# Performance work log

Hardware: AMD Instinct MI355X
Metric: run time of the kernel (lower is better)

## Reference

```python
import jax, jax.numpy as jnp
import numpy as np

B, T, I, H = 32768, 18, 2, 64  # batch, seq_len (forced by fc2 in_features=18), input_dim, hidden_dim


def setup_inputs() -> dict:
    key = jax.random.key(0)
    ks = jax.random.split(key, 13)
    s = 1.0 / np.sqrt(H)  # torch default GRU/Linear init scale
    return {
        "x": jax.random.normal(ks[0], (B, T, I), jnp.float32),
        "w_ih_f": jax.random.uniform(ks[1], (3 * H, I), jnp.float32, -s, s),
        "w_hh_f": jax.random.uniform(ks[2], (3 * H, H), jnp.float32, -s, s),
        "b_ih_f": jax.random.uniform(ks[3], (3 * H,), jnp.float32, -s, s),
        "b_hh_f": jax.random.uniform(ks[4], (3 * H,), jnp.float32, -s, s),
        "w_ih_b": jax.random.uniform(ks[5], (3 * H, I), jnp.float32, -s, s),
        "w_hh_b": jax.random.uniform(ks[6], (3 * H, H), jnp.float32, -s, s),
        "b_ih_b": jax.random.uniform(ks[7], (3 * H,), jnp.float32, -s, s),
        "b_hh_b": jax.random.uniform(ks[8], (3 * H,), jnp.float32, -s, s),
        "fc1_w": jax.random.uniform(ks[9], (24, 2 * H), jnp.float32, -s, s),
        "fc1_b": jax.random.uniform(ks[10], (24,), jnp.float32, -s, s),
        "fc2_w": jax.random.uniform(ks[11], (2, T), jnp.float32, -s, s),
        "fc2_b": jax.random.uniform(ks[12], (2,), jnp.float32, -s, s),
    }


def _gru_scan(x_proj, w_hh, b_hh):
    """x_proj: (T, B, 3H) precomputed input projections. Returns (T, B, H)."""
    h0 = jnp.zeros((x_proj.shape[1], w_hh.shape[1]), x_proj.dtype)

    def step(h, xp):
        gh = h @ w_hh.T + b_hh
        i_r, i_z, i_n = jnp.split(xp, 3, axis=-1)
        h_r, h_z, h_n = jnp.split(gh, 3, axis=-1)
        r = jax.nn.sigmoid(i_r + h_r)
        z = jax.nn.sigmoid(i_z + h_z)
        n = jnp.tanh(i_n + r * h_n)
        h_new = (1 - z) * n + z * h
        return h_new, h_new

    _, hs = jax.lax.scan(step, h0, x_proj)
    return hs


def reference(x, w_ih_f, w_hh_f, b_ih_f, b_hh_f,
              w_ih_b, w_hh_b, b_ih_b, b_hh_b,
              fc1_w, fc1_b, fc2_w, fc2_b):
    # precompute input-gate projections for both directions: (T, B, 3H)
    xp_f = jnp.einsum('bti,gi->tbg', x, w_ih_f) + b_ih_f
    xp_b = jnp.einsum('bti,gi->tbg', x[:, ::-1], w_ih_b) + b_ih_b
    hf = _gru_scan(xp_f, w_hh_f, b_hh_f)           # (T, B, H)
    hb = _gru_scan(xp_b, w_hh_b, b_hh_b)[::-1]     # (T, B, H), re-aligned to forward time
    out = jnp.concatenate([hf, hb], axis=-1).transpose(1, 0, 2)  # (B, T, 2H)
    out = out @ fc1_w.T + fc1_b                    # (B, T, 24)
    out = out.reshape(out.shape[0], 24, -1)        # (B, 24, T) raw row-major reshape, as in torch
    out = out @ fc2_w.T + fc2_b                    # (B, 24, 2)
    return out
```

## Files before the change

### kernel.cpp

```cpp
#include <hip/hip_runtime.h>

#define TT 18

typedef __attribute__((ext_vector_type(8))) short short8;
typedef __attribute__((ext_vector_type(4))) float float4_t;
typedef __attribute__((ext_vector_type(2))) unsigned int uint2_t;

#if defined(__has_builtin)
#if __has_builtin(__builtin_amdgcn_exp2f)
#define FEXP2(x) __builtin_amdgcn_exp2f(x)
#else
#define FEXP2(x) exp2f(x)
#endif
#else
#define FEXP2(x) exp2f(x)
#endif

static __device__ __forceinline__ float frcp(float x){ return __builtin_amdgcn_rcpf(x); }
static __device__ __forceinline__ unsigned rne_bits(float f){
    unsigned u = __float_as_uint(f);
    return u + 0x7fffu + ((u >> 16) & 1u);
}
static __device__ __forceinline__ void bsplit(float f, unsigned &hi, unsigned &lo){
    unsigned rb = rne_bits(f);
    hi = rb >> 16;
    float fh = __uint_as_float(rb & 0xffff0000u);
    lo = rne_bits(f - fh) >> 16;
}
static __device__ __forceinline__ unsigned pack_hi16(unsigned hi_src, unsigned lo_src){
#if defined(__has_builtin)
#if __has_builtin(__builtin_amdgcn_perm)
    return __builtin_amdgcn_perm(hi_src, lo_src, 0x07060302u);
#else
    return (lo_src >> 16) | (hi_src & 0xffff0000u);
#endif
#else
    return (lo_src >> 16) | (hi_src & 0xffff0000u);
#endif
}

union U8 { short8 s; unsigned u[4]; };

#define MFMA16(A,B,C) __builtin_amdgcn_mfma_f32_16x16x32_bf16((A),(B),(C),0,0,0)

__global__ __launch_bounds__(256) void head_precompute(
    const float* __restrict__ fc1_w, const float* __restrict__ fc1_b,
    const float* __restrict__ fc2_w, const float* __restrict__ fc2_b,
    unsigned short* __restrict__ Bhi, unsigned short* __restrict__ Blo,
    float* __restrict__ Cvec)
{
    int idx = blockIdx.x * 256 + threadIdx.x;
    if (idx < 24 * 2 * 18 * 128) {
        int jg = idx & 127;
        int t  = (idx >> 7) % 18;
        int k  = (idx / 2304) & 1;
        int r  = idx / 4608;
        float acc = 0.f;
        for (int c = 0; c < 24; ++c) {
            int s = t * 24 + c - r * 18;
            if (s >= 0 && s < 18) acc += fc2_w[k * 18 + s] * fc1_w[c * 128 + jg];
        }
        unsigned hi, lo;
        bsplit(acc, hi, lo);
        Bhi[idx] = (unsigned short)hi;
        Blo[idx] = (unsigned short)lo;
    }
    if (idx < 48) {
        int k = idx & 1, r = idx >> 1;
        float acc = fc2_b[k];
        for (int s = 0; s < 18; ++s)
            acc += fc2_w[k * 18 + s] * fc1_b[(r * 18 + s) % 24];
        Cvec[idx] = acc;
    }
}

struct SMv {
    alignas(16) unsigned short hb[2][2][1024];
    alignas(16) unsigned short b2x[2][64][8];
    alignas(16) unsigned short c2a[4][4][16][8];
    alignas(16) unsigned short zero16[8];
    uint2_t x2[16][18];
    float out_acc[16][49];
};

__global__ __launch_bounds__(256, 4) void gru_mfma(
    const float* __restrict__ x,
    const float* __restrict__ w_ih_f, const float* __restrict__ w_hh_f,
    const float* __restrict__ b_ih_f, const float* __restrict__ b_hh_f,
    const float* __restrict__ w_ih_b, const float* __restrict__ w_hh_b,
    const float* __restrict__ b_ih_b, const float* __restrict__ b_hh_b,
    const unsigned short* __restrict__ Bhi, const unsigned short* __restrict__ Blo,
    const float* __restrict__ Cvec, float* __restrict__ out)
{
    __shared__ SMv sm;
    const int tid  = threadIdx.x;
    const int lane = tid & 63;
    const int jq   = tid >> 6;
    const int col  = lane & 15;
    const int quad = lane >> 4;
    const int bi   = blockIdx.x;
    const int dir  = bi >> 11;
    const int bb   = (bi & 2047) * 16;
    const bool q0  = (quad == 0);

    const float* __restrict__ wih = dir ? w_ih_b : w_ih_f;
    const float* __restrict__ whh = dir ? w_hh_b : w_hh_f;
    const float* __restrict__ bih = dir ? b_ih_b : b_ih_f;
    const float* __restrict__ bhh = dir ? b_hh_b : b_hh_f;

    const float L1 = 1.4426950408889634f;
    const float L2 = 2.8853900817779268f;

    {
        unsigned* z = (unsigned*)&sm.hb[1][0][0];
        #pragma unroll
        for (int o = 0; o < 4; ++o) z[tid + o * 256] = 0u;
        unsigned* z2 = (unsigned*)&sm.b2x[0][0][0];
        #pragma unroll
        for (int o = 0; o < 2; ++o) z2[tid + o * 256] = 0u;
        if (tid < 4) ((unsigned*)sm.zero16)[tid] = 0u;
    }
    for (int o = tid; o < 16 * 49; o += 256) ((float*)sm.out_acc)[o] = 0.f;

    for (int p = tid; p < 288; p += 256) {
        int b = p / 18, t = p % 18;
        const float* xp = x + (size_t)(bb + b) * 36 + t * 2;
        unsigned h0, l0, h1, l1;
        bsplit(xp[0], h0, l0);
        bsplit(xp[1], h1, l1);
        uint2_t s2; s2[0] = h0 | (l0 << 16); s2[1] = h1 | (l1 << 16);
        sm.x2[b][t] = s2;
    }

    if (tid < 16) {
        int tx0 = dir ? (TT - 1) : 0;
        const float* xp = x + (size_t)(bb + tid) * 36 + tx0 * 2;
        unsigned h0, l0, h1, l1;
        bsplit(xp[0], h0, l0);
        bsplit(xp[1], h1, l1);
        U8 B;
        B.u[0] = h0 | (l0 << 16);
        B.u[1] = h0 | (h1 << 16);
        B.u[2] = l1 | (h1 << 16);
        B.u[3] = 0x3F803F80u;
        *(short8*)&sm.b2x[1][tid][0] = B.s;
    }

    if (q0) {
        int g0 = jq * 16 + col;
        #pragma unroll
        for (int ty = 0; ty < 2; ++ty) {
            int g = ty * 64 + g0;
            unsigned w0h, w0l, w1h, w1l, bh, bl;
            bsplit(L1 * wih[2 * g],     w0h, w0l);
            bsplit(L1 * wih[2 * g + 1], w1h, w1l);
            bsplit(L1 * (bih[g] + bhh[g]), bh, bl);
            U8 f;
            f.u[0] = w0h | (w0h << 16);
            f.u[1] = w0l | (w1h << 16);
            f.u[2] = w1h | (w1l << 16);
            f.u[3] = bh  | (bl  << 16);
            *(short8*)&sm.c2a[jq][ty][col][0] = f.s;
        }
        {
            unsigned bh, bl;
            bsplit(L2 * bhh[128 + g0], bh, bl);
            U8 f;
            f.u[0] = 0u; f.u[1] = 0u; f.u[2] = 0u;
            f.u[3] = bh | (bl << 16);
            *(short8*)&sm.c2a[jq][2][col][0] = f.s;
        }
        {
            int g = 128 + g0;
            unsigned w0h, w0l, w1h, w1l, bh, bl;
            bsplit(L2 * wih[2 * g],     w0h, w0l);
            bsplit(L2 * wih[2 * g + 1], w1h, w1l);
            bsplit(L2 * bih[g], bh, bl);
            U8 f;
            f.u[0] = w0h | (w0h << 16);
            f.u[1] = w0l | (w1h << 16);
            f.u[2] = w1h | (w1l << 16);
            f.u[3] = bh  | (bl  << 16);
            *(short8*)&sm.c2a[jq][3][col][0] = f.s;
        }
    }

    short8 wf[3][2];
    #pragma unroll
    for (int ty = 0; ty < 3; ++ty) {
        float sc = (ty == 2) ? L2 : L1;
        int g = ty * 64 + jq * 16 + col;
        #pragma unroll
        for (int c = 0; c < 2; ++c) {
            const float* p = whh + g * 64 + c * 32 + quad * 8;
            float4_t f0 = *(const float4_t*)p;
            float4_t f1 = *(const float4_t*)(p + 4);
            short8 s;
            #pragma unroll
            for (int e = 0; e < 8; ++e) {
                float f = (e < 4) ? f0[e] : f1[e - 4];
                s[e] = (short)(rne_bits(sc * f) >> 16);
            }
            wf[ty][c] = s;
        }
    }

    const unsigned short* c2p0 = q0 ? &sm.c2a[jq][0][col][0] : sm.zero16;
    const unsigned short* c2p1 = q0 ? &sm.c2a[jq][1][col][0] : sm.zero16;
    const unsigned short* c2p2 = q0 ? &sm.c2a[jq][2][col][0] : sm.zero16;
    const unsigned short* c2p3 = q0 ? &sm.c2a[jq][3][col][0] : sm.zero16;

    float hprev[4] = {0.f, 0.f, 0.f, 0.f};

    __syncthreads();

    auto step = [&](int t, int pr, int pw) {
        short8 hfh[2];
        hfh[0] = *(const short8*)&sm.hb[pr][0][quad * 128 + col * 8];
        hfh[1] = *(const short8*)&sm.hb[pr][0][(4 + quad) * 128 + col * 8];
        short8 b2f  = *(const short8*)&sm.b2x[pr][lane][0];
        short8 c2f0 = *(const short8*)c2p0;
        short8 c2f1 = *(const short8*)c2p1;
        short8 c2f2 = *(const short8*)c2p2;
        short8 c2f3 = *(const short8*)c2p3;

        float4_t aR  = (float4_t){0.f,0.f,0.f,0.f};
        float4_t aZ  = (float4_t){0.f,0.f,0.f,0.f};
        float4_t aNH = (float4_t){0.f,0.f,0.f,0.f};
        float4_t aNX = (float4_t){0.f,0.f,0.f,0.f};
        aR  = MFMA16(wf[0][0], hfh[0], aR);
        aR  = MFMA16(wf[0][1], hfh[1], aR);
        aR  = MFMA16(c2f0,     b2f,    aR);
        aZ  = MFMA16(wf[1][0], hfh[0], aZ);
        aZ  = MFMA16(wf[1][1], hfh[1], aZ);
        aZ  = MFMA16(c2f1,     b2f,    aZ);
        aNH = MFMA16(wf[2][0], hfh[0], aNH);
        aNH = MFMA16(wf[2][1], hfh[1], aNH);
        aNH = MFMA16(c2f2,     b2f,    aNH);
        aNX = MFMA16(c2f3,     b2f,    aNX);

        unsigned rh[4], rl[4];
        #pragma unroll
        for (int reg = 0; reg < 4; ++reg) {
            float r = frcp(1.f + FEXP2(-aR[reg]));
            float z = frcp(1.f + FEXP2(-aZ[reg]));
            float a = fmaf(r, aNH[reg], aNX[reg]);
            float n = fmaf(2.f, frcp(1.f + FEXP2(-a)), -1.f);
            float hnew = fmaf(z, hprev[reg] - n, n);
            hprev[reg] = hnew;
            unsigned rb = rne_bits(hnew);
            rh[reg] = rb;
            rl[reg] = __float_as_uint(hnew - __uint_as_float(rb & 0xffff0000u));
        }
        int woff = (jq * 2 + (quad >> 1)) * 128 + col * 8 + (quad & 1) * 4;
        uint2_t dh, dl;
        dh[0] = pack_hi16(rh[1], rh[0]);
        dh[1] = pack_hi16(rh[3], rh[2]);
        dl[0] = pack_hi16(rl[1], rl[0]);
        dl[1] = pack_hi16(rl[3], rl[2]);
        *(uint2_t*)&sm.hb[pw][0][woff] = dh;
        *(uint2_t*)&sm.hb[pw][1][woff] = dl;

        if (jq == 0 && q0) {
            int tn  = (t + 1 < TT) ? (t + 1) : (TT - 1);
            int txn = dir ? (TT - 1 - tn) : tn;
            uint2_t xs = sm.x2[col][txn];
            U8 B;
            B.u[0] = xs[0];
            B.u[1] = (xs[0] & 0xffffu) | (xs[1] << 16);
            B.u[2] = (xs[1] >> 16) | (xs[1] << 16);
            B.u[3] = 0x3F803F80u;
            *(short8*)&sm.b2x[pw][lane][0] = B.s;
        }

        if (t > 0 && ((t - 1) & 3) == jq) {
            int s  = t - 1;
            int ta = dir ? (TT - 1 - s) : s;
            int base_h = 4 * (ta / 3) + ta % 3;
            int i  = col & 3;
            int rr = base_h + (i >> 1);
            int kk = i & 1;
            size_t boff = (size_t)((rr * 2 + kk) * TT + ta) * 128 + dir * 64 + quad * 8;
            short8 hA0 = *(const short8*)(Bhi + boff);
            short8 hA1 = *(const short8*)(Bhi + boff + 32);
            short8 lA0 = *(const short8*)(Blo + boff);
            short8 lA1 = *(const short8*)(Blo + boff + 32);
            short8 hfl0 = *(const short8*)&sm.hb[pr][1][quad * 128 + col * 8];
            short8 hfl1 = *(const short8*)&sm.hb[pr][1][(4 + quad) * 128 + col * 8];
            float4_t acch = (float4_t){0.f,0.f,0.f,0.f};
            acch = MFMA16(hA0, hfh[0], acch);
            acch = MFMA16(hA1, hfh[1], acch);
            acch = MFMA16(hA0, hfl0,   acch);
            acch = MFMA16(hA1, hfl1,   acch);
            acch = MFMA16(lA0, hfh[0], acch);
            acch = MFMA16(lA1, hfh[1], acch);
            if (q0) {
                #pragma unroll
                for (int reg = 0; reg < 4; ++reg) {
                    int r2 = base_h + (reg >> 1);
                    sm.out_acc[col][r2 * 2 + (reg & 1)] += acch[reg];
                }
            }
        }
        __syncthreads();
    };

    #pragma unroll 1
    for (int tt = 0; tt < 9; ++tt) {
        step(2 * tt,     1, 0);
        step(2 * tt + 1, 0, 1);
    }

    if (jq == ((TT - 1) & 3)) {
        int s  = TT - 1;
        int ta = dir ? 0 : s;
        int base_h = 4 * (ta / 3) + ta % 3;
        int i  = col & 3;
        int rr = base_h + (i >> 1);
        int kk = i & 1;
        size_t boff = (size_t)((rr * 2 + kk) * TT + ta) * 128 + dir * 64 + quad * 8;
        short8 hA0 = *(const short8*)(Bhi + boff);
        short8 hA1 = *(const short8*)(Bhi + boff + 32);
        short8 lA0 = *(const short8*)(Blo + boff);
        short8 lA1 = *(const short8*)(Blo + boff + 32);
        short8 hfh0 = *(const short8*)&sm.hb[1][0][quad * 128 + col * 8];
        short8 hfh1 = *(const short8*)&sm.hb[1][0][(4 + quad) * 128 + col * 8];
        short8 hfl0 = *(const short8*)&sm.hb[1][1][quad * 128 + col * 8];
        short8 hfl1 = *(const short8*)&sm.hb[1][1][(4 + quad) * 128 + col * 8];
        float4_t acch = (float4_t){0.f,0.f,0.f,0.f};
        acch = MFMA16(hA0, hfh0, acch);
        acch = MFMA16(hA1, hfh1, acch);
        acch = MFMA16(hA0, hfl0, acch);
        acch = MFMA16(hA1, hfl1, acch);
        acch = MFMA16(lA0, hfh0, acch);
        acch = MFMA16(lA1, hfh1, acch);
        if (q0) {
            #pragma unroll
            for (int reg = 0; reg < 4; ++reg) {
                int r2 = base_h + (reg >> 1);
                sm.out_acc[col][r2 * 2 + (reg & 1)] += acch[reg];
            }
        }
    }
    __syncthreads();

    #pragma unroll
    for (int rep = 0; rep < 3; ++rep) {
        int o = rep * 256 + tid;
        int b = o / 48, c = o % 48;
        atomicAdd(&out[(size_t)bb * 48 + o], sm.out_acc[b][c] + 0.5f * Cvec[c]);
    }
}

extern "C" void kernel_launch(void* const* d_in, const int* in_sizes, int n_in,
                              void* d_out, int out_size, void* d_ws, size_t ws_size,
                              hipStream_t stream) {
    const float* x      = (const float*)d_in[0];
    const float* w_ih_f = (const float*)d_in[1];
    const float* w_hh_f = (const float*)d_in[2];
    const float* b_ih_f = (const float*)d_in[3];
    const float* b_hh_f = (const float*)d_in[4];
    const float* w_ih_b = (const float*)d_in[5];
    const float* w_hh_b = (const float*)d_in[6];
    const float* b_ih_b = (const float*)d_in[7];
    const float* b_hh_b = (const float*)d_in[8];
    const float* fc1_w  = (const float*)d_in[9];
    const float* fc1_b  = (const float*)d_in[10];
    const float* fc2_w  = (const float*)d_in[11];
    const float* fc2_b  = (const float*)d_in[12];
    float* out  = (float*)d_out;

    float*          Cvec = (float*)d_ws;
    unsigned short* Bhi  = (unsigned short*)((char*)d_ws + 256);
    unsigned short* Blo  = Bhi + 110592;

    hipMemsetAsync(d_out, 0, (size_t)out_size * sizeof(float), stream);
    head_precompute<<<432, 256, 0, stream>>>(fc1_w, fc1_b, fc2_w, fc2_b, Bhi, Blo, Cvec);
    gru_mfma<<<4096, 256, 0, stream>>>(x, w_ih_f, w_hh_f, b_ih_f, b_hh_f,
                                       w_ih_b, w_hh_b, b_ih_b, b_hh_b,
                                       Bhi, Blo, Cvec, out);
}
```

Measured before the change: 193.6 us.

## Fuse both GRU directions per block, process 32 batch rows, drop atomics and memset

Each block now runs both directions (8 waves, 4 per direction) over 32 batch rows, with each wave handling two 16-column MFMA tiles per step. Input x is kept as fp32 in shared memory and split to bf16 hi/lo on the fly, and the gate input weights move from shared memory into registers. Per-direction partial outputs are summed in shared memory and written directly, which removes the atomicAdd and the output memset. The cost is higher register and LDS pressure per block, and occupancy may drop under 512-thread launch bounds.

```diff
diff --git a/kernel.cpp b/kernel.cpp
--- a/kernel.cpp
+++ b/kernel.cpp
@@ -4,6 +4,7 @@
 
 typedef __attribute__((ext_vector_type(8))) short short8;
 typedef __attribute__((ext_vector_type(4))) float float4_t;
+typedef __attribute__((ext_vector_type(2))) float float2_t;
 typedef __attribute__((ext_vector_type(2))) unsigned int uint2_t;
 
 #if defined(__has_builtin)
@@ -42,6 +43,18 @@
 union U8 { short8 s; unsigned u[4]; };
 
 #define MFMA16(A,B,C) __builtin_amdgcn_mfma_f32_16x16x32_bf16((A),(B),(C),0,0,0)
+
+static __device__ __forceinline__ short8 make_b2f(float x0, float x1, bool q0){
+    unsigned h0, l0, h1, l1;
+    bsplit(x0, h0, l0);
+    bsplit(x1, h1, l1);
+    U8 B;
+    B.u[0] = q0 ? (h0 | (l0 << 16)) : 0u;
+    B.u[1] = q0 ? (h0 | (h1 << 16)) : 0u;
+    B.u[2] = q0 ? (l1 | (h1 << 16)) : 0u;
+    B.u[3] = q0 ? 0x3F803F80u : 0u;
+    return B.s;
+}
 
 __global__ __launch_bounds__(256) void head_precompute(
     const float* __restrict__ fc1_w, const float* __restrict__ fc1_b,
@@ -75,15 +88,12 @@
 }
 
 struct SMv {
-    alignas(16) unsigned short hb[2][2][1024];
-    alignas(16) unsigned short b2x[2][64][8];
-    alignas(16) unsigned short c2a[4][4][16][8];
-    alignas(16) unsigned short zero16[8];
-    uint2_t x2[16][18];
-    float out_acc[16][49];
+    alignas(16) unsigned short hb[2][2][2][2048];
+    float2_t x_s[32][18];
+    float out_acc[2][32][49];
 };
 
-__global__ __launch_bounds__(256, 4) void gru_mfma(
+__global__ __launch_bounds__(512, 4) void gru_mfma(
     const float* __restrict__ x,
     const float* __restrict__ w_ih_f, const float* __restrict__ w_hh_f,
     const float* __restrict__ b_ih_f, const float* __restrict__ b_hh_f,
@@ -95,12 +105,12 @@
     __shared__ SMv sm;
     const int tid  = threadIdx.x;
     const int lane = tid & 63;
-    const int jq   = tid >> 6;
+    const int wave = tid >> 6;
+    const int dir  = wave >> 2;
+    const int jq   = wave & 3;
     const int col  = lane & 15;
     const int quad = lane >> 4;
-    const int bi   = blockIdx.x;
-    const int dir  = bi >> 11;
-    const int bb   = (bi & 2047) * 16;
+    const int bb   = blockIdx.x * 32;
     const bool q0  = (quad == 0);
 
     const float* __restrict__ wih = dir ? w_ih_b : w_ih_f;
@@ -112,77 +122,15 @@
     const float L2 = 2.8853900817779268f;
 
     {
-        unsigned* z = (unsigned*)&sm.hb[1][0][0];
-        #pragma unroll
-        for (int o = 0; o < 4; ++o) z[tid + o * 256] = 0u;
-        unsigned* z2 = (unsigned*)&sm.b2x[0][0][0];
-        #pragma unroll
-        for (int o = 0; o < 2; ++o) z2[tid + o * 256] = 0u;
-        if (tid < 4) ((unsigned*)sm.zero16)[tid] = 0u;
-    }
-    for (int o = tid; o < 16 * 49; o += 256) ((float*)sm.out_acc)[o] = 0.f;
-
-    for (int p = tid; p < 288; p += 256) {
+        unsigned* z = (unsigned*)&sm.hb[1][0][0][0];
+        #pragma unroll
+        for (int o = 0; o < 8; ++o) z[tid + o * 512] = 0u;
+    }
+    for (int o = tid; o < 2 * 32 * 49; o += 512) ((float*)sm.out_acc)[o] = 0.f;
+
+    for (int p = tid; p < 32 * 18; p += 512) {
         int b = p / 18, t = p % 18;
-        const float* xp = x + (size_t)(bb + b) * 36 + t * 2;
-        unsigned h0, l0, h1, l1;
-        bsplit(xp[0], h0, l0);
-        bsplit(xp[1], h1, l1);
-        uint2_t s2; s2[0] = h0 | (l0 << 16); s2[1] = h1 | (l1 << 16);
-        sm.x2[b][t] = s2;
-    }
-
-    if (tid < 16) {
-        int tx0 = dir ? (TT - 1) : 0;
-        const float* xp = x + (size_t)(bb + tid) * 36 + tx0 * 2;
-        unsigned h0, l0, h1, l1;
-        bsplit(xp[0], h0, l0);
-        bsplit(xp[1], h1, l1);
-        U8 B;
-        B.u[0] = h0 | (l0 << 16);
-        B.u[1] = h0 | (h1 << 16);
-        B.u[2] = l1 | (h1 << 16);
-        B.u[3] = 0x3F803F80u;
-        *(short8*)&sm.b2x[1][tid][0] = B.s;
-    }
-
-    if (q0) {
-        int g0 = jq * 16 + col;
-        #pragma unroll
-        for (int ty = 0; ty < 2; ++ty) {
-            int g = ty * 64 + g0;
-            unsigned w0h, w0l, w1h, w1l, bh, bl;
-            bsplit(L1 * wih[2 * g],     w0h, w0l);
-            bsplit(L1 * wih[2 * g + 1], w1h, w1l);
-            bsplit(L1 * (bih[g] + bhh[g]), bh, bl);
-            U8 f;
-            f.u[0] = w0h | (w0h << 16);
-            f.u[1] = w0l | (w1h << 16);
-            f.u[2] = w1h | (w1l << 16);
-            f.u[3] = bh  | (bl  << 16);
-            *(short8*)&sm.c2a[jq][ty][col][0] = f.s;
-        }
-        {
-            unsigned bh, bl;
-            bsplit(L2 * bhh[128 + g0], bh, bl);
-            U8 f;
-            f.u[0] = 0u; f.u[1] = 0u; f.u[2] = 0u;
-            f.u[3] = bh | (bl << 16);
-            *(short8*)&sm.c2a[jq][2][col][0] = f.s;
-        }
-        {
-            int g = 128 + g0;
-            unsigned w0h, w0l, w1h, w1l, bh, bl;
-            bsplit(L2 * wih[2 * g],     w0h, w0l);
-            bsplit(L2 * wih[2 * g + 1], w1h, w1l);
-            bsplit(L2 * bih[g], bh, bl);
-            U8 f;
-            f.u[0] = w0h | (w0h << 16);
-            f.u[1] = w0l | (w1h << 16);
-            f.u[2] = w1h | (w1l << 16);
-            f.u[3] = bh  | (bl  << 16);
-            *(short8*)&sm.c2a[jq][3][col][0] = f.s;
-        }
+        sm.x_s[b][t] = *(const float2_t*)(x + (size_t)(bb + b) * 36 + t * 2);
     }
 
     short8 wf[3][2];
@@ -205,103 +153,152 @@
         }
     }
 
-    const unsigned short* c2p0 = q0 ? &sm.c2a[jq][0][col][0] : sm.zero16;
-    const unsigned short* c2p1 = q0 ? &sm.c2a[jq][1][col][0] : sm.zero16;
-    const unsigned short* c2p2 = q0 ? &sm.c2a[jq][2][col][0] : sm.zero16;
-    const unsigned short* c2p3 = q0 ? &sm.c2a[jq][3][col][0] : sm.zero16;
-
-    float hprev[4] = {0.f, 0.f, 0.f, 0.f};
+    short8 c2[4];
+    {
+        int g0 = jq * 16 + col;
+        #pragma unroll
+        for (int ty = 0; ty < 2; ++ty) {
+            int g = ty * 64 + g0;
+            unsigned w0h, w0l, w1h, w1l, bh, bl;
+            bsplit(L1 * wih[2 * g],     w0h, w0l);
+            bsplit(L1 * wih[2 * g + 1], w1h, w1l);
+            bsplit(L1 * (bih[g] + bhh[g]), bh, bl);
+            U8 f;
+            f.u[0] = q0 ? (w0h | (w0h << 16)) : 0u;
+            f.u[1] = q0 ? (w0l | (w1h << 16)) : 0u;
+            f.u[2] = q0 ? (w1h | (w1l << 16)) : 0u;
+            f.u[3] = q0 ? (bh  | (bl  << 16)) : 0u;
+            c2[ty] = f.s;
+        }
+        {
+            unsigned bh, bl;
+            bsplit(L2 * bhh[128 + g0], bh, bl);
+            U8 f;
+            f.u[0] = 0u; f.u[1] = 0u; f.u[2] = 0u;
+            f.u[3] = q0 ? (bh | (bl << 16)) : 0u;
+            c2[2] = f.s;
+        }
+        {
+            int g = 128 + g0;
+            unsigned w0h, w0l, w1h, w1l, bh, bl;
+            bsplit(L2 * wih[2 * g],     w0h, w0l);
+            bsplit(L2 * wih[2 * g + 1], w1h, w1l);
+            bsplit(L2 * bih[g], bh, bl);
+            U8 f;
+            f.u[0] = q0 ? (w0h | (w0h << 16)) : 0u;
+            f.u[1] = q0 ? (w0l | (w1h << 16)) : 0u;
+            f.u[2] = q0 ? (w1h | (w1l << 16)) : 0u;
+            f.u[3] = q0 ? (bh  | (bl  << 16)) : 0u;
+            c2[3] = f.s;
+        }
+    }
+
+    float hprev[8] = {0.f,0.f,0.f,0.f,0.f,0.f,0.f,0.f};
 
     __syncthreads();
 
     auto step = [&](int t, int pr, int pw) {
-        short8 hfh[2];
-        hfh[0] = *(const short8*)&sm.hb[pr][0][quad * 128 + col * 8];
-        hfh[1] = *(const short8*)&sm.hb[pr][0][(4 + quad) * 128 + col * 8];
-        short8 b2f  = *(const short8*)&sm.b2x[pr][lane][0];
-        short8 c2f0 = *(const short8*)c2p0;
-        short8 c2f1 = *(const short8*)c2p1;
-        short8 c2f2 = *(const short8*)c2p2;
-        short8 c2f3 = *(const short8*)c2p3;
-
-        float4_t aR  = (float4_t){0.f,0.f,0.f,0.f};
-        float4_t aZ  = (float4_t){0.f,0.f,0.f,0.f};
-        float4_t aNH = (float4_t){0.f,0.f,0.f,0.f};
-        float4_t aNX = (float4_t){0.f,0.f,0.f,0.f};
-        aR  = MFMA16(wf[0][0], hfh[0], aR);
-        aR  = MFMA16(wf[0][1], hfh[1], aR);
-        aR  = MFMA16(c2f0,     b2f,    aR);
-        aZ  = MFMA16(wf[1][0], hfh[0], aZ);
-        aZ  = MFMA16(wf[1][1], hfh[1], aZ);
-        aZ  = MFMA16(c2f1,     b2f,    aZ);
-        aNH = MFMA16(wf[2][0], hfh[0], aNH);
-        aNH = MFMA16(wf[2][1], hfh[1], aNH);
-        aNH = MFMA16(c2f2,     b2f,    aNH);
-        aNX = MFMA16(c2f3,     b2f,    aNX);
-
-        unsigned rh[4], rl[4];
-        #pragma unroll
-        for (int reg = 0; reg < 4; ++reg) {
-            float r = frcp(1.f + FEXP2(-aR[reg]));
-            float z = frcp(1.f + FEXP2(-aZ[reg]));
-            float a = fmaf(r, aNH[reg], aNX[reg]);
-            float n = fmaf(2.f, frcp(1.f + FEXP2(-a)), -1.f);
-            float hnew = fmaf(z, hprev[reg] - n, n);
-            hprev[reg] = hnew;
-            unsigned rb = rne_bits(hnew);
-            rh[reg] = rb;
-            rl[reg] = __float_as_uint(hnew - __uint_as_float(rb & 0xffff0000u));
-        }
-        int woff = (jq * 2 + (quad >> 1)) * 128 + col * 8 + (quad & 1) * 4;
-        uint2_t dh, dl;
-        dh[0] = pack_hi16(rh[1], rh[0]);
-        dh[1] = pack_hi16(rh[3], rh[2]);
-        dl[0] = pack_hi16(rl[1], rl[0]);
-        dl[1] = pack_hi16(rl[3], rl[2]);
-        *(uint2_t*)&sm.hb[pw][0][woff] = dh;
-        *(uint2_t*)&sm.hb[pw][1][woff] = dl;
-
-        if (jq == 0 && q0) {
-            int tn  = (t + 1 < TT) ? (t + 1) : (TT - 1);
-            int txn = dir ? (TT - 1 - tn) : tn;
-            uint2_t xs = sm.x2[col][txn];
-            U8 B;
-            B.u[0] = xs[0];
-            B.u[1] = (xs[0] & 0xffffu) | (xs[1] << 16);
-            B.u[2] = (xs[1] >> 16) | (xs[1] << 16);
-            B.u[3] = 0x3F803F80u;
-            *(short8*)&sm.b2x[pw][lane][0] = B.s;
-        }
-
-        if (t > 0 && ((t - 1) & 3) == jq) {
+        const bool myturn = (t > 0) && (((t - 1) & 3) == jq);
+        const int tx = dir ? (TT - 1 - t) : t;
+
+        short8 h0c0 = *(const short8*)&sm.hb[pr][dir][0][quad * 256 + col * 8];
+        short8 h0c1 = *(const short8*)&sm.hb[pr][dir][0][(4 + quad) * 256 + col * 8];
+        short8 h1c0 = *(const short8*)&sm.hb[pr][dir][0][quad * 256 + (16 + col) * 8];
+        short8 h1c1 = *(const short8*)&sm.hb[pr][dir][0][(4 + quad) * 256 + (16 + col) * 8];
+
+        float2_t xv0 = sm.x_s[col][tx];
+        float2_t xv1 = sm.x_s[16 + col][tx];
+        short8 b2f0 = make_b2f(xv0[0], xv0[1], q0);
+        short8 b2f1 = make_b2f(xv1[0], xv1[1], q0);
+
+        short8 hA0, hA1, lA0, lA1, l0c0, l0c1, l1c0, l1c1;
+        int base_h = 0;
+        if (myturn) {
             int s  = t - 1;
             int ta = dir ? (TT - 1 - s) : s;
-            int base_h = 4 * (ta / 3) + ta % 3;
+            base_h = 4 * (ta / 3) + ta % 3;
             int i  = col & 3;
             int rr = base_h + (i >> 1);
             int kk = i & 1;
             size_t boff = (size_t)((rr * 2 + kk) * TT + ta) * 128 + dir * 64 + quad * 8;
-            short8 hA0 = *(const short8*)(Bhi + boff);
-            short8 hA1 = *(const short8*)(Bhi + boff + 32);
-            short8 lA0 = *(const short8*)(Blo + boff);
-            short8 lA1 = *(const short8*)(Blo + boff + 32);
-            short8 hfl0 = *(const short8*)&sm.hb[pr][1][quad * 128 + col * 8];
-            short8 hfl1 = *(const short8*)&sm.hb[pr][1][(4 + quad) * 128 + col * 8];
-            float4_t acch = (float4_t){0.f,0.f,0.f,0.f};
-            acch = MFMA16(hA0, hfh[0], acch);
-            acch = MFMA16(hA1, hfh[1], acch);
-            acch = MFMA16(hA0, hfl0,   acch);
-            acch = MFMA16(hA1, hfl1,   acch);
-            acch = MFMA16(lA0, hfh[0], acch);
-            acch = MFMA16(lA1, hfh[1], acch);
-            if (q0) {
-                #pragma unroll
-                for (int reg = 0; reg < 4; ++reg) {
-                    int r2 = base_h + (reg >> 1);
-                    sm.out_acc[col][r2 * 2 + (reg & 1)] += acch[reg];
+            hA0 = *(const short8*)(Bhi + boff);
+            hA1 = *(const short8*)(Bhi + boff + 32);
+            lA0 = *(const short8*)(Blo + boff);
+            lA1 = *(const short8*)(Blo + boff + 32);
+            l0c0 = *(const short8*)&sm.hb[pr][dir][1][quad * 256 + col * 8];
+            l0c1 = *(const short8*)&sm.hb[pr][dir][1][(4 + quad) * 256 + col * 8];
+            l1c0 = *(const short8*)&sm.hb[pr][dir][1][quad * 256 + (16 + col) * 8];
+            l1c1 = *(const short8*)&sm.hb[pr][dir][1][(4 + quad) * 256 + (16 + col) * 8];
+        }
+
+        #pragma unroll
+        for (int nt = 0; nt < 2; ++nt) {
+            short8 hc0 = nt ? h1c0 : h0c0;
+            short8 hc1 = nt ? h1c1 : h0c1;
+            short8 b2f = nt ? b2f1 : b2f0;
+            float4_t aR  = (float4_t){0.f,0.f,0.f,0.f};
+            float4_t aZ  = (float4_t){0.f,0.f,0.f,0.f};
+            float4_t aNH = (float4_t){0.f,0.f,0.f,0.f};
+            float4_t aNX = (float4_t){0.f,0.f,0.f,0.f};
+            aR  = MFMA16(wf[0][0], hc0, aR);
+            aR  = MFMA16(wf[0][1], hc1, aR);
+            aR  = MFMA16(c2[0],    b2f, aR);
+            aZ  = MFMA16(wf[1][0], hc0, aZ);
+            aZ  = MFMA16(wf[1][1], hc1, aZ);
+            aZ  = MFMA16(c2[1],    b2f, aZ);
+            aNH = MFMA16(wf[2][0], hc0, aNH);
+            aNH = MFMA16(wf[2][1], hc1, aNH);
+            aNH = MFMA16(c2[2],    b2f, aNH);
+            aNX = MFMA16(c2[3],    b2f, aNX);
+
+            unsigned rh[4], rl[4];
+            #pragma unroll
+            for (int reg = 0; reg < 4; ++reg) {
+                float r = frcp(1.f + FEXP2(-aR[reg]));
+                float z = frcp(1.f + FEXP2(-aZ[reg]));
+                float a = fmaf(r, aNH[reg], aNX[reg]);
+                float n = fmaf(2.f, frcp(1.f + FEXP2(-a)), -1.f);
+                float hnew = fmaf(z, hprev[nt * 4 + reg] - n, n);
+                hprev[nt * 4 + reg] = hnew;
+                unsigned rb = rne_bits(hnew);
+                rh[reg] = rb;
+                rl[reg] = __float_as_uint(hnew - __uint_as_float(rb & 0xffff0000u));
+            }
+            int woff = (jq * 2 + (quad >> 1)) * 256 + (nt * 16 + col) * 8 + (quad & 1) * 4;
+            uint2_t dh, dl;
+            dh[0] = pack_hi16(rh[1], rh[0]);
+            dh[1] = pack_hi16(rh[3], rh[2]);
+            dl[0] = pack_hi16(rl[1], rl[0]);
+            dl[1] = pack_hi16(rl[3], rl[2]);
+            *(uint2_t*)&sm.hb[pw][dir][0][woff] = dh;
+            *(uint2_t*)&sm.hb[pw][dir][1][woff] = dl;
+
+            if (nt == 0 && myturn) {
+                float4_t a0 = (float4_t){0.f,0.f,0.f,0.f};
+                a0 = MFMA16(hA0, h0c0, a0);
+                a0 = MFMA16(hA1, h0c1, a0);
+                a0 = MFMA16(hA0, l0c0, a0);
+                a0 = MFMA16(hA1, l0c1, a0);
+                a0 = MFMA16(lA0, h0c0, a0);
+                a0 = MFMA16(lA1, h0c1, a0);
+                float4_t a1 = (float4_t){0.f,0.f,0.f,0.f};
+                a1 = MFMA16(hA0, h1c0, a1);
+                a1 = MFMA16(hA1, h1c1, a1);
+                a1 = MFMA16(hA0, l1c0, a1);
+                a1 = MFMA16(hA1, l1c1, a1);
+                a1 = MFMA16(lA0, h1c0, a1);
+                a1 = MFMA16(lA1, h1c1, a1);
+                if (q0) {
+                    #pragma unroll
+                    for (int reg = 0; reg < 4; ++reg) {
+                        int cell = (base_h + (reg >> 1)) * 2 + (reg & 1);
+                        sm.out_acc[dir][col][cell]      += a0[reg];
+                        sm.out_acc[dir][16 + col][cell] += a1[reg];
+                    }
                 }
             }
         }
+
         __syncthreads();
     };
 
@@ -323,22 +320,25 @@
         short8 hA1 = *(const short8*)(Bhi + boff + 32);
         short8 lA0 = *(const short8*)(Blo + boff);
         short8 lA1 = *(const short8*)(Blo + boff + 32);
-        short8 hfh0 = *(const short8*)&sm.hb[1][0][quad * 128 + col * 8];
-        short8 hfh1 = *(const short8*)&sm.hb[1][0][(4 + quad) * 128 + col * 8];
-        short8 hfl0 = *(const short8*)&sm.hb[1][1][quad * 128 + col * 8];
-        short8 hfl1 = *(const short8*)&sm.hb[1][1][(4 + quad) * 128 + col * 8];
-        float4_t acch = (float4_t){0.f,0.f,0.f,0.f};
-        acch = MFMA16(hA0, hfh0, acch);
-        acch = MFMA16(hA1, hfh1, acch);
-        acch = MFMA16(hA0, hfl0, acch);
-        acch = MFMA16(hA1, hfl1, acch);
-        acch = MFMA16(lA0, hfh0, acch);
-        acch = MFMA16(lA1, hfh1, acch);
-        if (q0) {
-            #pragma unroll
-            for (int reg = 0; reg < 4; ++reg) {
-                int r2 = base_h + (reg >> 1);
-                sm.out_acc[col][r2 * 2 + (reg & 1)] += acch[reg];
+        #pragma unroll
+        for (int nt = 0; nt < 2; ++nt) {
+            short8 hc0 = *(const short8*)&sm.hb[1][dir][0][quad * 256 + (nt * 16 + col) * 8];
+            short8 hc1 = *(const short8*)&sm.hb[1][dir][0][(4 + quad) * 256 + (nt * 16 + col) * 8];
+            short8 lc0 = *(const short8*)&sm.hb[1][dir][1][quad * 256 + (nt * 16 + col) * 8];
+            short8 lc1 = *(const short8*)&sm.hb[1][dir][1][(4 + quad) * 256 + (nt * 16 + col) * 8];
+            float4_t acch = (float4_t){0.f,0.f,0.f,0.f};
+            acch = MFMA16(hA0, hc0, acch);
+            acch = MFMA16(hA1, hc1, acch);
+            acch = MFMA16(hA0, lc0, acch);
+            acch = MFMA16(hA1, lc1, acch);
+            acch = MFMA16(lA0, hc0, acch);
+            acch = MFMA16(lA1, hc1, acch);
+            if (q0) {
+                #pragma unroll
+                for (int reg = 0; reg < 4; ++reg) {
+                    int cell = (base_h + (reg >> 1)) * 2 + (reg & 1);
+                    sm.out_acc[dir][nt * 16 + col][cell] += acch[reg];
+                }
             }
         }
     }
@@ -346,9 +346,9 @@
 
     #pragma unroll
     for (int rep = 0; rep < 3; ++rep) {
-        int o = rep * 256 + tid;
+        int o = rep * 512 + tid;
         int b = o / 48, c = o % 48;
-        atomicAdd(&out[(size_t)bb * 48 + o], sm.out_acc[b][c] + 0.5f * Cvec[c]);
+        out[(size_t)bb * 48 + o] = sm.out_acc[0][b][c] + sm.out_acc[1][b][c] + Cvec[c];
     }
 }
 
@@ -374,9 +374,8 @@
     unsigned short* Bhi  = (unsigned short*)((char*)d_ws + 256);
     unsigned short* Blo  = Bhi + 110592;
 
-    hipMemsetAsync(d_out, 0, (size_t)out_size * sizeof(float), stream);
     head_precompute<<<432, 256, 0, stream>>>(fc1_w, fc1_b, fc2_w, fc2_b, Bhi, Blo, Cvec);
-    gru_mfma<<<4096, 256, 0, stream>>>(x, w_ih_f, w_hh_f, b_ih_f, b_hh_f,
+    gru_mfma<<<1024, 512, 0, stream>>>(x, w_ih_f, w_hh_f, b_ih_f, b_hh_f,
                                        w_ih_b, w_hh_b, b_ih_b, b_hh_b,
                                        Bhi, Blo, Cvec, out);
 }
```

Measured after the change: 181.6 us. 1.07x faster.
